# Kernel tuning notes

Measured on AMD Instinct MI355X. Metric: run time of the kernel, lower is better.

The kernel has to match this reference:

```python
import jax, jax.numpy as jnp
import numpy as np

B, T, D, H, W = 512, 4096, 8, 16, 16  # batch, timesteps, data_size, hidden_size, width_size


def lipswish(x):
    return 0.909 * jax.nn.silu(x)


def _linear_params(key, out_f, in_f):
    kw, kb = jax.random.split(key)
    lim = 1.0 / np.sqrt(in_f)
    w = jax.random.uniform(kw, (out_f, in_f), minval=-lim, maxval=lim, dtype=jnp.float32)
    b = jax.random.uniform(kb, (out_f,), minval=-lim, maxval=lim, dtype=jnp.float32)
    return w, b


def setup_inputs() -> dict:
    key = jax.random.key(0)
    ks = jax.random.split(key, 9)
    ts = jnp.arange(T, dtype=jnp.float32)
    ys = jax.random.normal(ks[0], (B, T, D), dtype=jnp.float32)
    # initial MLP: (D+1) -> W -> H, relu hidden, identity final
    iW1, ib1 = _linear_params(ks[1], W, D + 1)
    iW2, ib2 = _linear_params(ks[2], H, W)
    # vf MLP: (H+1) -> W -> H, lipswish hidden, tanh final; scale=False -> ones (identity)
    vW1, vb1 = _linear_params(ks[3], W, H + 1)
    vW2, vb2 = _linear_params(ks[4], H, W)
    # cvf MLP: (H+1) -> W -> H*D, lipswish hidden, tanh final; scale=False -> ones
    cW1, cb1 = _linear_params(ks[5], W, H + 1)
    cW2, cb2 = _linear_params(ks[6], H * D, W)
    # readout: H -> 1
    rW, rb = _linear_params(ks[7], 1, H)
    return dict(ts=ts, ys=ys, iW1=iW1, ib1=ib1, iW2=iW2, ib2=ib2,
                vW1=vW1, vb1=vb1, vW2=vW2, vb2=vb2,
                cW1=cW1, cb1=cb1, cW2=cW2, cb2=cb2, rW=rW, rb=rb)


def reference(ts, ys, iW1, ib1, iW2, ib2, vW1, vb1, vW2, vb2,
              cW1, cb1, cW2, cb2, rW, rb):
    Bn, Tn, Dn = ys.shape
    Hn = iW2.shape[0]
    # initial hidden state: initial MLP on concat([t0, y0])
    init_in = jnp.concatenate([jnp.broadcast_to(ts[0], (Bn, 1)), ys[:, 0]], axis=1)  # (B, D+1)
    y0 = jax.nn.relu(init_in @ iW1.T + ib1) @ iW2.T + ib2  # (B, H)
    # Euler with dt=1 on integer-spaced ts: control increment = ys[n+1]-ys[n]
    dX = jnp.swapaxes(ys[:, 1:] - ys[:, :-1], 0, 1)  # (T-1, B, D)
    t_steps = ts[0] + jnp.arange(Tn - 1, dtype=ys.dtype)  # (T-1,)

    def step(y, inp):
        t, dx = inp  # scalar, (B, D)
        z = jnp.concatenate([jnp.broadcast_to(t, (Bn, 1)), y], axis=1)  # (B, H+1)
        f = jnp.tanh(lipswish(z @ vW1.T + vb1) @ vW2.T + vb2)           # (B, H) drift
        g = jnp.tanh(lipswish(z @ cW1.T + cb1) @ cW2.T + cb2)           # (B, H*D)
        g = g.reshape(Bn, Hn, Dn)
        y = y + f + jnp.einsum('bhd,bd->bh', g, dx)  # dt = 1.0
        return y, None

    yT, _ = jax.lax.scan(step, y0, (t_steps, dX))
    saved = jnp.stack([y0, yT], axis=1)  # SaveAt(t0=True, t1=True) -> (B, 2, H)
    return saved @ rW.T + rb  # (B, 2, 1)
```

## Files before the change

### kernel.cpp

```cpp
#include <hip/hip_runtime.h>

#define T_LEN 4096

typedef float v2f __attribute__((ext_vector_type(2)));

__device__ __forceinline__ float frcp(float x) { return __builtin_amdgcn_rcpf(x); }
__device__ __forceinline__ float fexp2(float x) { return __builtin_amdgcn_exp2f(x); }

__device__ __forceinline__ float rl(float v, int lane) {
  return __int_as_float(__builtin_amdgcn_readlane(__float_as_int(v), lane));
}
__device__ __forceinline__ float rfl(float v) {
  return __int_as_float(__builtin_amdgcn_readfirstlane(__float_as_int(v)));
}

__device__ __forceinline__ void pk_fma_s(v2f& acc, v2f w, v2f s) {
  asm("v_pk_fma_f32 %0, %1, %2, %0" : "+v"(acc) : "v"(w), "s"(s));
}

template <int CTRL>
__device__ __forceinline__ float dpp_add(float x) {
  int t = __builtin_amdgcn_mov_dpp(__float_as_int(x), CTRL, 0xF, 0xF, true);
  return x + __int_as_float(t);
}

__global__ __launch_bounds__(64) void disc_kernel(
    const float* __restrict__ ts, const float* __restrict__ ys,
    const float* __restrict__ iW1, const float* __restrict__ ib1,
    const float* __restrict__ iW2, const float* __restrict__ ib2,
    const float* __restrict__ vW1, const float* __restrict__ vb1,
    const float* __restrict__ vW2, const float* __restrict__ vb2,
    const float* __restrict__ cW1, const float* __restrict__ cb1,
    const float* __restrict__ cW2, const float* __restrict__ cb2,
    const float* __restrict__ rW, const float* __restrict__ rb,
    float* __restrict__ out)
{
  const int b   = blockIdx.x;
  const int l   = threadIdx.x;
  const int h16 = l & 15;
  const int p   = (l >> 4) & 1;
  const int hf  = l >> 2;
  const int d0  = (2 * l) & 7;

  __shared__ __align__(16) float sbuf[16];
  __shared__ __align__(16) float ybuf[16];
  __shared__ __align__(16) float xbuf[1024];

  const float* __restrict__ ysb = ys + (size_t)b * (T_LEN * 8);

  const float NL2E = -1.4426950408889634f;
  const float TSW  = 2.0f * 1.4426950408889634f * 0.909f;
  const float TSB  = 2.0f * 1.4426950408889634f;
  const float NLN2 = -0.6931471805599453f;

  float w1t, b1m;
  v2f W1y2[8];
  {
    const float* W1 = p ? cW1 : vW1;
    const float* bv = p ? cb1 : vb1;
    w1t = NL2E * W1[h16 * 17];
    b1m = NL2E * bv[h16];
#pragma unroll
    for (int k = 0; k < 8; ++k) {
      v2f w; w.x = NL2E * W1[h16 * 17 + 1 + 2 * k];
             w.y = NL2E * W1[h16 * 17 + 2 + 2 * k];
      W1y2[k] = w;
    }
  }
  v2f W2p[8], G0p[8], G1p[8];
#pragma unroll
  for (int k = 0; k < 8; ++k) {
    v2f a; a.x = TSW * vW2[hf * 16 + 2 * k]; a.y = TSW * vW2[hf * 16 + 2 * k + 1];
    W2p[k] = a;
    v2f c0; c0.x = TSW * cW2[(2 * l) * 16 + 2 * k]; c0.y = TSW * cW2[(2 * l) * 16 + 2 * k + 1];
    G0p[k] = c0;
    v2f c1; c1.x = TSW * cW2[(2 * l + 1) * 16 + 2 * k]; c1.y = TSW * cW2[(2 * l + 1) * 16 + 2 * k + 1];
    G1p[k] = c1;
  }
  const float b2p  = TSB * vb2[hf];
  const float bg0p = TSB * cb2[2 * l];
  const float bg1p = TSB * cb2[2 * l + 1];

  const float t0 = ts[0];

  float y_own;
  v2f yu2[8];
  {
    float acc = ib1[h16] + iW1[h16 * 9] * t0;
#pragma unroll
    for (int d = 0; d < 8; ++d) acc = fmaf(iW1[h16 * 9 + 1 + d], ysb[d], acc);
    acc = fmaxf(acc, 0.0f);
    sbuf[h16] = acc;
    float acc2 = ib2[h16];
#pragma unroll
    for (int k = 0; k < 16; ++k) acc2 = fmaf(iW2[h16 * 16 + k], sbuf[k], acc2);
    ybuf[h16] = acc2;
    y_own = ybuf[hf];
#pragma unroll
    for (int k = 0; k < 8; ++k) {
      v2f r; r.x = rfl(ybuf[2 * k]); r.y = rfl(ybuf[2 * k + 1]);
      yu2[k] = r;
    }
  }

  {
    float o = rb[0];
#pragma unroll
    for (int k = 0; k < 8; ++k) {
      o = fmaf(rW[2 * k], yu2[k].x, o);
      o = fmaf(rW[2 * k + 1], yu2[k].y, o);
    }
    if (l == 0) out[2 * b] = o;
  }

  const int CLAMP = T_LEN * 8 - 4;
  float4 A, Bq, Cq, Dq;
  {
    const int f0 = l * 8;
    A  = *(const float4*)(ysb + min(f0,      CLAMP));
    Bq = *(const float4*)(ysb + min(f0 + 4,  CLAMP));
    Cq = *(const float4*)(ysb + min(f0 + 8,  CLAMP));
    Dq = *(const float4*)(ysb + min(f0 + 12, CLAMP));
    float4 e0, e1;
    e0.x = Cq.x - A.x;  e0.y = Cq.y - A.y;  e0.z = Cq.z - A.z;  e0.w = Cq.w - A.w;
    e1.x = Dq.x - Bq.x; e1.y = Dq.y - Bq.y; e1.z = Dq.z - Bq.z; e1.w = Dq.w - Bq.w;
    *(float4*)(xbuf + l * 8)     = e0;
    *(float4*)(xbuf + l * 8 + 4) = e1;
  }

  float t = t0;
  for (int c = 0; c < 64; ++c) {
    {
      const int cn = min(c + 1, 63);
      const int f0 = cn * 512 + l * 8;
      A  = *(const float4*)(ysb + min(f0,      CLAMP));
      Bq = *(const float4*)(ysb + min(f0 + 4,  CLAMP));
      Cq = *(const float4*)(ysb + min(f0 + 8,  CLAMP));
      Dq = *(const float4*)(ysb + min(f0 + 12, CLAMP));
    }
    const float* __restrict__ xb = xbuf + (c & 1) * 512;
    const int base = c * 64;
    const int nsteps = min(64, (T_LEN - 1) - base);
    for (int j = 0; j < nsteps; ++j) {
      const v2f dx = *(const v2f*)(xb + j * 8 + d0);

      const float m_t = fmaf(w1t, t, b1m);
      v2f ma; ma.x = m_t; ma.y = 0.0f;
      v2f mb; mb.x = 0.0f; mb.y = 0.0f;
#pragma unroll
      for (int k = 0; k < 4; ++k) {
        pk_fma_s(ma, W1y2[k], yu2[k]);
        pk_fma_s(mb, W1y2[4 + k], yu2[4 + k]);
      }
      const v2f ms = ma + mb;
      const float m = ms.x + ms.y;
      const float eM = fexp2(m);
      const float u  = m * NLN2;
      const float s  = u * frcp(1.0f + eM);

      v2f su2[16];
#pragma unroll
      for (int k = 8; k < 16; ++k) {
        v2f r; r.x = rl(s, 2 * k); r.y = rl(s, 2 * k + 1);
        su2[k] = r;
      }
      v2f ga; ga.x = bg0p; ga.y = 0.0f;
      v2f gc; gc.x = 0.0f; gc.y = 0.0f;
      v2f gb; gb.x = bg1p; gb.y = 0.0f;
      v2f gd; gd.x = 0.0f; gd.y = 0.0f;
#pragma unroll
      for (int k = 0; k < 4; ++k) {
        pk_fma_s(ga, G0p[k],     su2[8 + k]);
        pk_fma_s(gc, G0p[4 + k], su2[12 + k]);
        pk_fma_s(gb, G1p[k],     su2[8 + k]);
        pk_fma_s(gd, G1p[4 + k], su2[12 + k]);
      }
#pragma unroll
      for (int k = 0; k < 8; ++k) {
        v2f r; r.x = rl(s, 2 * k); r.y = rl(s, 2 * k + 1);
        su2[k] = r;
      }
      v2f fa; fa.x = b2p; fa.y = 0.0f;
      v2f fb; fb.x = 0.0f; fb.y = 0.0f;
#pragma unroll
      for (int k = 0; k < 4; ++k) {
        pk_fma_s(fa, W2p[k],     su2[k]);
        pk_fma_s(fb, W2p[4 + k], su2[4 + k]);
      }

      const v2f gs0 = ga + gc;
      const v2f gs1 = gb + gd;
      const float g0v = fmaf(-2.0f, frcp(1.0f + fexp2(gs0.x + gs0.y)), 1.0f);
      const float g1v = fmaf(-2.0f, frcp(1.0f + fexp2(gs1.x + gs1.y)), 1.0f);
      const v2f fs = fa + fb;
      const float fv = fmaf(-2.0f, frcp(1.0f + fexp2(fs.x + fs.y)), 1.0f);

      float pr = fmaf(g0v, dx.x, g1v * dx.y);
      pr = dpp_add<0xB1>(pr);
      pr = dpp_add<0x4E>(pr);

      y_own = y_own + (fv + pr);
#pragma unroll
      for (int k = 0; k < 8; ++k) {
        v2f r; r.x = rl(y_own, 8 * k); r.y = rl(y_own, 8 * k + 4);
        yu2[k] = r;
      }
      t += 1.0f;
    }
    float* xbn = xbuf + ((c + 1) & 1) * 512;
    float4 e0, e1;
    e0.x = Cq.x - A.x;  e0.y = Cq.y - A.y;  e0.z = Cq.z - A.z;  e0.w = Cq.w - A.w;
    e1.x = Dq.x - Bq.x; e1.y = Dq.y - Bq.y; e1.z = Dq.z - Bq.z; e1.w = Dq.w - Bq.w;
    *(float4*)(xbn + l * 8)     = e0;
    *(float4*)(xbn + l * 8 + 4) = e1;
  }

  {
    float o = rb[0];
#pragma unroll
    for (int k = 0; k < 8; ++k) {
      o = fmaf(rW[2 * k], yu2[k].x, o);
      o = fmaf(rW[2 * k + 1], yu2[k].y, o);
    }
    if (l == 0) out[2 * b + 1] = o;
  }
}

extern "C" void kernel_launch(void* const* d_in, const int* in_sizes, int n_in,
                              void* d_out, int out_size, void* d_ws, size_t ws_size,
                              hipStream_t stream) {
  (void)in_sizes; (void)n_in; (void)out_size; (void)d_ws; (void)ws_size;
  const float* ts  = (const float*)d_in[0];
  const float* ys  = (const float*)d_in[1];
  const float* iW1 = (const float*)d_in[2];
  const float* ib1 = (const float*)d_in[3];
  const float* iW2 = (const float*)d_in[4];
  const float* ib2 = (const float*)d_in[5];
  const float* vW1 = (const float*)d_in[6];
  const float* vb1 = (const float*)d_in[7];
  const float* vW2 = (const float*)d_in[8];
  const float* vb2 = (const float*)d_in[9];
  const float* cW1 = (const float*)d_in[10];
  const float* cb1 = (const float*)d_in[11];
  const float* cW2 = (const float*)d_in[12];
  const float* cb2 = (const float*)d_in[13];
  const float* rW  = (const float*)d_in[14];
  const float* rb  = (const float*)d_in[15];
  float* out = (float*)d_out;
  hipLaunchKernelGGL(disc_kernel, dim3(512), dim3(64), 0, stream,
                     ts, ys, iW1, ib1, iW2, ib2, vW1, vb1, vW2, vb2,
                     cW1, cb1, cW2, cb2, rW, rb, out);
}
```

Baseline: 1.220 ms.

## Interleave two batch elements per wavefront to raise instruction-level parallelism

Each 64-lane block now integrates two independent batch trajectories, A and B, side by side. Their per-step MLP evaluations, readlane broadcasts and DPP reductions are interleaved so the two dependency chains can hide each other's latency. The shared-memory increment buffer is re-laid out to hold both elements' dx values in one float4 per lane. The grid halves to 256 blocks, so fewer waves run concurrently and each wave does twice the arithmetic per step. That may cost more than it saves if the original was not purely latency-bound.

```diff
diff --git a/kernel.cpp b/kernel.cpp
--- a/kernel.cpp
+++ b/kernel.cpp
@@ -22,6 +22,10 @@
 __device__ __forceinline__ float dpp_add(float x) {
   int t = __builtin_amdgcn_mov_dpp(__float_as_int(x), CTRL, 0xF, 0xF, true);
   return x + __int_as_float(t);
+}
+
+__device__ __forceinline__ float tanh_pre(float x) {
+  return fmaf(-2.0f, frcp(1.0f + fexp2(x)), 1.0f);
 }
 
 __global__ __launch_bounds__(64) void disc_kernel(
@@ -35,18 +39,20 @@
     const float* __restrict__ rW, const float* __restrict__ rb,
     float* __restrict__ out)
 {
-  const int b   = blockIdx.x;
-  const int l   = threadIdx.x;
-  const int h16 = l & 15;
-  const int p   = (l >> 4) & 1;
-  const int hf  = l >> 2;
-  const int d0  = (2 * l) & 7;
-
-  __shared__ __align__(16) float sbuf[16];
-  __shared__ __align__(16) float ybuf[16];
-  __shared__ __align__(16) float xbuf[1024];
-
-  const float* __restrict__ ysb = ys + (size_t)b * (T_LEN * 8);
+  const int b    = blockIdx.x;
+  const int l    = threadIdx.x;
+  const int h16  = l & 15;
+  const int p    = (l >> 4) & 1;
+  const int hf   = l >> 2;
+  const int d0   = (2 * l) & 7;
+  const int dblk = d0 >> 1;
+
+  __shared__ __align__(16) float sbuf[32];
+  __shared__ __align__(16) float ybuf[32];
+  __shared__ __align__(16) float xbuf[2048];
+
+  const float* __restrict__ ysA = ys + (size_t)(2 * b)     * (T_LEN * 8);
+  const float* __restrict__ ysB = ys + (size_t)(2 * b + 1) * (T_LEN * 8);
 
   const float NL2E = -1.4426950408889634f;
   const float TSW  = 2.0f * 1.4426950408889634f * 0.909f;
@@ -83,146 +89,186 @@
 
   const float t0 = ts[0];
 
-  float y_own;
-  v2f yu2[8];
-  {
-    float acc = ib1[h16] + iW1[h16 * 9] * t0;
-#pragma unroll
-    for (int d = 0; d < 8; ++d) acc = fmaf(iW1[h16 * 9 + 1 + d], ysb[d], acc);
-    acc = fmaxf(acc, 0.0f);
-    sbuf[h16] = acc;
-    float acc2 = ib2[h16];
-#pragma unroll
-    for (int k = 0; k < 16; ++k) acc2 = fmaf(iW2[h16 * 16 + k], sbuf[k], acc2);
-    ybuf[h16] = acc2;
-    y_own = ybuf[hf];
-#pragma unroll
-    for (int k = 0; k < 8; ++k) {
-      v2f r; r.x = rfl(ybuf[2 * k]); r.y = rfl(ybuf[2 * k + 1]);
-      yu2[k] = r;
-    }
-  }
-
-  {
-    float o = rb[0];
-#pragma unroll
-    for (int k = 0; k < 8; ++k) {
-      o = fmaf(rW[2 * k], yu2[k].x, o);
-      o = fmaf(rW[2 * k + 1], yu2[k].y, o);
-    }
-    if (l == 0) out[2 * b] = o;
+  float y_ownA, y_ownB;
+  v2f yuA[8], yuB[8];
+  {
+    float accA = ib1[h16] + iW1[h16 * 9] * t0;
+    float accB = accA;
+#pragma unroll
+    for (int d = 0; d < 8; ++d) {
+      accA = fmaf(iW1[h16 * 9 + 1 + d], ysA[d], accA);
+      accB = fmaf(iW1[h16 * 9 + 1 + d], ysB[d], accB);
+    }
+    sbuf[h16]      = fmaxf(accA, 0.0f);
+    sbuf[16 + h16] = fmaxf(accB, 0.0f);
+    float y2A = ib2[h16], y2B = ib2[h16];
+#pragma unroll
+    for (int k = 0; k < 16; ++k) {
+      y2A = fmaf(iW2[h16 * 16 + k], sbuf[k],      y2A);
+      y2B = fmaf(iW2[h16 * 16 + k], sbuf[16 + k], y2B);
+    }
+    ybuf[h16]      = y2A;
+    ybuf[16 + h16] = y2B;
+    y_ownA = ybuf[hf];
+    y_ownB = ybuf[16 + hf];
+#pragma unroll
+    for (int k = 0; k < 8; ++k) {
+      v2f rA; rA.x = rfl(ybuf[2 * k]);      rA.y = rfl(ybuf[2 * k + 1]);
+      v2f rB; rB.x = rfl(ybuf[16 + 2 * k]); rB.y = rfl(ybuf[16 + 2 * k + 1]);
+      yuA[k] = rA; yuB[k] = rB;
+    }
+  }
+
+  {
+    float oA = rb[0], oB = rb[0];
+#pragma unroll
+    for (int k = 0; k < 8; ++k) {
+      oA = fmaf(rW[2 * k], yuA[k].x, oA); oA = fmaf(rW[2 * k + 1], yuA[k].y, oA);
+      oB = fmaf(rW[2 * k], yuB[k].x, oB); oB = fmaf(rW[2 * k + 1], yuB[k].y, oB);
+    }
+    if (l == 0) { out[4 * b] = oA; out[4 * b + 2] = oB; }
   }
 
   const int CLAMP = T_LEN * 8 - 4;
-  float4 A, Bq, Cq, Dq;
+
   {
     const int f0 = l * 8;
-    A  = *(const float4*)(ysb + min(f0,      CLAMP));
-    Bq = *(const float4*)(ysb + min(f0 + 4,  CLAMP));
-    Cq = *(const float4*)(ysb + min(f0 + 8,  CLAMP));
-    Dq = *(const float4*)(ysb + min(f0 + 12, CLAMP));
-    float4 e0, e1;
-    e0.x = Cq.x - A.x;  e0.y = Cq.y - A.y;  e0.z = Cq.z - A.z;  e0.w = Cq.w - A.w;
-    e1.x = Dq.x - Bq.x; e1.y = Dq.y - Bq.y; e1.z = Dq.z - Bq.z; e1.w = Dq.w - Bq.w;
-    *(float4*)(xbuf + l * 8)     = e0;
-    *(float4*)(xbuf + l * 8 + 4) = e1;
+    float4 a0 = *(const float4*)(ysA + f0);
+    float4 a1 = *(const float4*)(ysA + f0 + 4);
+    float4 a2 = *(const float4*)(ysA + f0 + 8);
+    float4 a3 = *(const float4*)(ysA + f0 + 12);
+    float4 b0 = *(const float4*)(ysB + f0);
+    float4 b1 = *(const float4*)(ysB + f0 + 4);
+    float4 b2 = *(const float4*)(ysB + f0 + 8);
+    float4 b3 = *(const float4*)(ysB + f0 + 12);
+    float4 dAlo, dAhi, dBlo, dBhi;
+    dAlo.x = a2.x - a0.x; dAlo.y = a2.y - a0.y; dAlo.z = a2.z - a0.z; dAlo.w = a2.w - a0.w;
+    dAhi.x = a3.x - a1.x; dAhi.y = a3.y - a1.y; dAhi.z = a3.z - a1.z; dAhi.w = a3.w - a1.w;
+    dBlo.x = b2.x - b0.x; dBlo.y = b2.y - b0.y; dBlo.z = b2.z - b0.z; dBlo.w = b2.w - b0.w;
+    dBhi.x = b3.x - b1.x; dBhi.y = b3.y - b1.y; dBhi.z = b3.z - b1.z; dBhi.w = b3.w - b1.w;
+    float* w = xbuf + l * 16;
+    float4 q;
+    q.x = dAlo.x; q.y = dAlo.y; q.z = dBlo.x; q.w = dBlo.y; *(float4*)(w)      = q;
+    q.x = dAlo.z; q.y = dAlo.w; q.z = dBlo.z; q.w = dBlo.w; *(float4*)(w + 4)  = q;
+    q.x = dAhi.x; q.y = dAhi.y; q.z = dBhi.x; q.w = dBhi.y; *(float4*)(w + 8)  = q;
+    q.x = dAhi.z; q.y = dAhi.w; q.z = dBhi.z; q.w = dBhi.w; *(float4*)(w + 12) = q;
   }
 
   float t = t0;
   for (int c = 0; c < 64; ++c) {
+    float4 pA0, pA1, pA2, pA3, pB0, pB1, pB2, pB3;
     {
       const int cn = min(c + 1, 63);
-      const int f0 = cn * 512 + l * 8;
-      A  = *(const float4*)(ysb + min(f0,      CLAMP));
-      Bq = *(const float4*)(ysb + min(f0 + 4,  CLAMP));
-      Cq = *(const float4*)(ysb + min(f0 + 8,  CLAMP));
-      Dq = *(const float4*)(ysb + min(f0 + 12, CLAMP));
-    }
-    const float* __restrict__ xb = xbuf + (c & 1) * 512;
+      const int f0 = (cn * 64 + l) * 8;
+      pA0 = *(const float4*)(ysA + min(f0,      CLAMP));
+      pA1 = *(const float4*)(ysA + min(f0 + 4,  CLAMP));
+      pA2 = *(const float4*)(ysA + min(f0 + 8,  CLAMP));
+      pA3 = *(const float4*)(ysA + min(f0 + 12, CLAMP));
+      pB0 = *(const float4*)(ysB + min(f0,      CLAMP));
+      pB1 = *(const float4*)(ysB + min(f0 + 4,  CLAMP));
+      pB2 = *(const float4*)(ysB + min(f0 + 8,  CLAMP));
+      pB3 = *(const float4*)(ysB + min(f0 + 12, CLAMP));
+    }
+    const float* __restrict__ xb = xbuf + (c & 1) * 1024;
     const int base = c * 64;
     const int nsteps = min(64, (T_LEN - 1) - base);
     for (int j = 0; j < nsteps; ++j) {
-      const v2f dx = *(const v2f*)(xb + j * 8 + d0);
-
-      const float m_t = fmaf(w1t, t, b1m);
-      v2f ma; ma.x = m_t; ma.y = 0.0f;
-      v2f mb; mb.x = 0.0f; mb.y = 0.0f;
+      const float4 dx4 = *(const float4*)(xb + j * 16 + 4 * dblk);
+
+      const float mt = fmaf(w1t, t, b1m);
+      v2f maA; maA.x = mt; maA.y = 0.0f;  v2f mbA; mbA.x = 0.0f; mbA.y = 0.0f;
+      v2f maB; maB.x = mt; maB.y = 0.0f;  v2f mbB; mbB.x = 0.0f; mbB.y = 0.0f;
 #pragma unroll
       for (int k = 0; k < 4; ++k) {
-        pk_fma_s(ma, W1y2[k], yu2[k]);
-        pk_fma_s(mb, W1y2[4 + k], yu2[4 + k]);
-      }
-      const v2f ms = ma + mb;
-      const float m = ms.x + ms.y;
-      const float eM = fexp2(m);
-      const float u  = m * NLN2;
-      const float s  = u * frcp(1.0f + eM);
-
-      v2f su2[16];
-#pragma unroll
-      for (int k = 8; k < 16; ++k) {
-        v2f r; r.x = rl(s, 2 * k); r.y = rl(s, 2 * k + 1);
-        su2[k] = r;
-      }
-      v2f ga; ga.x = bg0p; ga.y = 0.0f;
-      v2f gc; gc.x = 0.0f; gc.y = 0.0f;
-      v2f gb; gb.x = bg1p; gb.y = 0.0f;
-      v2f gd; gd.x = 0.0f; gd.y = 0.0f;
+        pk_fma_s(maA, W1y2[k],     yuA[k]);
+        pk_fma_s(maB, W1y2[k],     yuB[k]);
+        pk_fma_s(mbA, W1y2[4 + k], yuA[4 + k]);
+        pk_fma_s(mbB, W1y2[4 + k], yuB[4 + k]);
+      }
+      const v2f msA = maA + mbA;  const float mA = msA.x + msA.y;
+      const v2f msB = maB + mbB;  const float mB = msB.x + msB.y;
+
+      const float eA = fexp2(mA);
+      const float eB = fexp2(mB);
+      const float sA = (mA * NLN2) * frcp(1.0f + eA);
+      const float sB = (mB * NLN2) * frcp(1.0f + eB);
+
+      v2f gaA; gaA.x = bg0p; gaA.y = 0.0f;  v2f gcA; gcA.x = 0.0f; gcA.y = 0.0f;
+      v2f gbA; gbA.x = bg1p; gbA.y = 0.0f;  v2f gdA; gdA.x = 0.0f; gdA.y = 0.0f;
+      v2f gaB; gaB.x = bg0p; gaB.y = 0.0f;  v2f gcB; gcB.x = 0.0f; gcB.y = 0.0f;
+      v2f gbB; gbB.x = bg1p; gbB.y = 0.0f;  v2f gdB; gdB.x = 0.0f; gdB.y = 0.0f;
 #pragma unroll
       for (int k = 0; k < 4; ++k) {
-        pk_fma_s(ga, G0p[k],     su2[8 + k]);
-        pk_fma_s(gc, G0p[4 + k], su2[12 + k]);
-        pk_fma_s(gb, G1p[k],     su2[8 + k]);
-        pk_fma_s(gd, G1p[4 + k], su2[12 + k]);
-      }
+        v2f slA; slA.x = rl(sA, 16 + 2 * k); slA.y = rl(sA, 17 + 2 * k);
+        v2f shA; shA.x = rl(sA, 24 + 2 * k); shA.y = rl(sA, 25 + 2 * k);
+        v2f slB; slB.x = rl(sB, 16 + 2 * k); slB.y = rl(sB, 17 + 2 * k);
+        v2f shB; shB.x = rl(sB, 24 + 2 * k); shB.y = rl(sB, 25 + 2 * k);
+        pk_fma_s(gaA, G0p[k], slA);  pk_fma_s(gcA, G0p[4 + k], shA);
+        pk_fma_s(gbA, G1p[k], slA);  pk_fma_s(gdA, G1p[4 + k], shA);
+        pk_fma_s(gaB, G0p[k], slB);  pk_fma_s(gcB, G0p[4 + k], shB);
+        pk_fma_s(gbB, G1p[k], slB);  pk_fma_s(gdB, G1p[4 + k], shB);
+      }
+
+      v2f faA; faA.x = b2p; faA.y = 0.0f;  v2f fbA; fbA.x = 0.0f; fbA.y = 0.0f;
+      v2f faB; faB.x = b2p; faB.y = 0.0f;  v2f fbB; fbB.x = 0.0f; fbB.y = 0.0f;
+#pragma unroll
+      for (int k = 0; k < 4; ++k) {
+        v2f slA; slA.x = rl(sA, 2 * k);     slA.y = rl(sA, 2 * k + 1);
+        v2f shA; shA.x = rl(sA, 8 + 2 * k); shA.y = rl(sA, 9 + 2 * k);
+        v2f slB; slB.x = rl(sB, 2 * k);     slB.y = rl(sB, 2 * k + 1);
+        v2f shB; shB.x = rl(sB, 8 + 2 * k); shB.y = rl(sB, 9 + 2 * k);
+        pk_fma_s(faA, W2p[k], slA);  pk_fma_s(fbA, W2p[4 + k], shA);
+        pk_fma_s(faB, W2p[k], slB);  pk_fma_s(fbB, W2p[4 + k], shB);
+      }
+
+      const v2f gsA0 = gaA + gcA;  const v2f gsA1 = gbA + gdA;
+      const v2f gsB0 = gaB + gcB;  const v2f gsB1 = gbB + gdB;
+      const float g0A = tanh_pre(gsA0.x + gsA0.y);
+      const float g1A = tanh_pre(gsA1.x + gsA1.y);
+      const float g0B = tanh_pre(gsB0.x + gsB0.y);
+      const float g1B = tanh_pre(gsB1.x + gsB1.y);
+      const v2f fsA = faA + fbA;   const v2f fsB = faB + fbB;
+      const float fvA = tanh_pre(fsA.x + fsA.y);
+      const float fvB = tanh_pre(fsB.x + fsB.y);
+
+      float prA = fmaf(g0A, dx4.x, g1A * dx4.y);
+      float prB = fmaf(g0B, dx4.z, g1B * dx4.w);
+      prA = dpp_add<0xB1>(prA);  prA = dpp_add<0x4E>(prA);
+      prB = dpp_add<0xB1>(prB);  prB = dpp_add<0x4E>(prB);
+
+      y_ownA = y_ownA + (fvA + prA);
+      y_ownB = y_ownB + (fvB + prB);
 #pragma unroll
       for (int k = 0; k < 8; ++k) {
-        v2f r; r.x = rl(s, 2 * k); r.y = rl(s, 2 * k + 1);
-        su2[k] = r;
-      }
-      v2f fa; fa.x = b2p; fa.y = 0.0f;
-      v2f fb; fb.x = 0.0f; fb.y = 0.0f;
-#pragma unroll
-      for (int k = 0; k < 4; ++k) {
-        pk_fma_s(fa, W2p[k],     su2[k]);
-        pk_fma_s(fb, W2p[4 + k], su2[4 + k]);
-      }
-
-      const v2f gs0 = ga + gc;
-      const v2f gs1 = gb + gd;
-      const float g0v = fmaf(-2.0f, frcp(1.0f + fexp2(gs0.x + gs0.y)), 1.0f);
-      const float g1v = fmaf(-2.0f, frcp(1.0f + fexp2(gs1.x + gs1.y)), 1.0f);
-      const v2f fs = fa + fb;
-      const float fv = fmaf(-2.0f, frcp(1.0f + fexp2(fs.x + fs.y)), 1.0f);
-
-      float pr = fmaf(g0v, dx.x, g1v * dx.y);
-      pr = dpp_add<0xB1>(pr);
-      pr = dpp_add<0x4E>(pr);
-
-      y_own = y_own + (fv + pr);
-#pragma unroll
-      for (int k = 0; k < 8; ++k) {
-        v2f r; r.x = rl(y_own, 8 * k); r.y = rl(y_own, 8 * k + 4);
-        yu2[k] = r;
+        v2f rA; rA.x = rl(y_ownA, 8 * k); rA.y = rl(y_ownA, 8 * k + 4);
+        yuA[k] = rA;
+        v2f rB; rB.x = rl(y_ownB, 8 * k); rB.y = rl(y_ownB, 8 * k + 4);
+        yuB[k] = rB;
       }
       t += 1.0f;
     }
-    float* xbn = xbuf + ((c + 1) & 1) * 512;
-    float4 e0, e1;
-    e0.x = Cq.x - A.x;  e0.y = Cq.y - A.y;  e0.z = Cq.z - A.z;  e0.w = Cq.w - A.w;
-    e1.x = Dq.x - Bq.x; e1.y = Dq.y - Bq.y; e1.z = Dq.z - Bq.z; e1.w = Dq.w - Bq.w;
-    *(float4*)(xbn + l * 8)     = e0;
-    *(float4*)(xbn + l * 8 + 4) = e1;
-  }
-
-  {
-    float o = rb[0];
-#pragma unroll
-    for (int k = 0; k < 8; ++k) {
-      o = fmaf(rW[2 * k], yu2[k].x, o);
-      o = fmaf(rW[2 * k + 1], yu2[k].y, o);
-    }
-    if (l == 0) out[2 * b + 1] = o;
+    {
+      float* w = xbuf + ((c + 1) & 1) * 1024 + l * 16;
+      float4 q;
+      q.x = pA2.x - pA0.x; q.y = pA2.y - pA0.y; q.z = pB2.x - pB0.x; q.w = pB2.y - pB0.y;
+      *(float4*)(w) = q;
+      q.x = pA2.z - pA0.z; q.y = pA2.w - pA0.w; q.z = pB2.z - pB0.z; q.w = pB2.w - pB0.w;
+      *(float4*)(w + 4) = q;
+      q.x = pA3.x - pA1.x; q.y = pA3.y - pA1.y; q.z = pB3.x - pB1.x; q.w = pB3.y - pB1.y;
+      *(float4*)(w + 8) = q;
+      q.x = pA3.z - pA1.z; q.y = pA3.w - pA1.w; q.z = pB3.z - pB1.z; q.w = pB3.w - pB1.w;
+      *(float4*)(w + 12) = q;
+    }
+  }
+
+  {
+    float oA = rb[0], oB = rb[0];
+#pragma unroll
+    for (int k = 0; k < 8; ++k) {
+      oA = fmaf(rW[2 * k], yuA[k].x, oA); oA = fmaf(rW[2 * k + 1], yuA[k].y, oA);
+      oB = fmaf(rW[2 * k], yuB[k].x, oB); oB = fmaf(rW[2 * k + 1], yuB[k].y, oB);
+    }
+    if (l == 0) { out[4 * b + 1] = oA; out[4 * b + 3] = oB; }
   }
 }
 
@@ -247,7 +293,7 @@
   const float* rW  = (const float*)d_in[14];
   const float* rb  = (const float*)d_in[15];
   float* out = (float*)d_out;
-  hipLaunchKernelGGL(disc_kernel, dim3(512), dim3(64), 0, stream,
+  hipLaunchKernelGGL(disc_kernel, dim3(256), dim3(64), 0, stream,
                      ts, ys, iW1, ib1, iW2, ib2, vW1, vb1, vW2, vb2,
                      cW1, cb1, cW2, cb2, rW, rb, out);
 }
```

After: 2.193 ms. +79.7%, slower.
